# Performance work log

Measured on AMD Instinct MI355X. Metric: run time of the kernel, lower is better.

Reference implementation:

```python
import jax, jax.numpy as jnp
import numpy as np

H = 16
INPUT_DIM = 1024
FEATURE_DIM = 1024
HEAD_DIM = FEATURE_DIM // H


def setup_inputs() -> dict:
    key = jax.random.key(0)
    ks = jax.random.split(key, 12)
    B, S = 4, 2048
    s = 1.0 / np.sqrt(INPUT_DIM)
    inp = {
        "data": jax.random.normal(ks[0], (B, S, INPUT_DIM), dtype=jnp.float32),
        "context": jax.random.normal(ks[1], (B, S, INPUT_DIM), dtype=jnp.float32),
        "wq": jax.random.normal(ks[2], (INPUT_DIM, FEATURE_DIM), dtype=jnp.float32) * s,
        "bq": jnp.zeros((FEATURE_DIM,), dtype=jnp.float32),
        "wk": jax.random.normal(ks[3], (INPUT_DIM, FEATURE_DIM), dtype=jnp.float32) * s,
        "bk": jnp.zeros((FEATURE_DIM,), dtype=jnp.float32),
        "wv": jax.random.normal(ks[4], (INPUT_DIM, FEATURE_DIM), dtype=jnp.float32) * s,
        "bv": jnp.zeros((FEATURE_DIM,), dtype=jnp.float32),
        "wo": jax.random.normal(ks[5], (FEATURE_DIM, INPUT_DIM), dtype=jnp.float32) * s,
        "bo": jnp.zeros((INPUT_DIM,), dtype=jnp.float32),
    }
    return inp


def reference(data, context, wq, bq, wk, bk, wv, bv, wo, bo):
    B, S1, _ = data.shape
    S2 = context.shape[1]
    # QKV projections -> (B, H, S, head_dim)
    q = (data @ wq + bq).reshape(B, S1, H, HEAD_DIM).transpose(0, 2, 1, 3)
    k = (context @ wk + bk).reshape(B, S2, H, HEAD_DIM).transpose(0, 2, 1, 3)
    v = (context @ wv + bv).reshape(B, S2, H, HEAD_DIM).transpose(0, 2, 1, 3)
    scale = 1.0 / np.sqrt(HEAD_DIM).astype(np.float32)
    scores = jnp.einsum("bhqd,bhkd->bhqk", q, k) * scale  # (B,H,S1,S2)
    # causal mask (is_causal=True, S1>1): row >= col
    causal = jnp.arange(S1)[:, None] >= jnp.arange(S2)[None, :]
    scores = jnp.where(causal, scores, -jnp.inf)
    probs = jax.nn.softmax(scores, axis=-1)
    z = jnp.einsum("bhqk,bhkd->bhqd", probs, v)  # (B,H,S1,head_dim)
    z = z.transpose(0, 2, 1, 3).reshape(B, S1, FEATURE_DIM)
    return z @ wo + bo
```

## Files before the change

kernel.cpp:

```cpp
#include <hip/hip_runtime.h>
#include <hip/hip_bf16.h>
#include <math.h>

typedef short  short8  __attribute__((ext_vector_type(8)));
typedef short  short4_ __attribute__((ext_vector_type(4)));
typedef float  f32x4   __attribute__((ext_vector_type(4)));

__device__ __forceinline__ unsigned short f2bf(float f) {
  unsigned int u = __float_as_uint(f);
  u += 0x7fffu + ((u >> 16) & 1u);
  return (unsigned short)(u >> 16);
}

__device__ __forceinline__ float fexp2(float x) {
  float r;
  asm("v_exp_f32 %0, %1" : "=v"(r) : "v"(x));
  return r;
}

__device__ __forceinline__ void load_lds16(const void* g, void* l) {
  __builtin_amdgcn_global_load_lds(
      (const __attribute__((address_space(1))) unsigned int*)g,
      (__attribute__((address_space(3))) unsigned int*)l, 16, 0, 0);
}

__device__ __forceinline__ void store_out(float* p, float v) { *p = v; }
__device__ __forceinline__ void store_out(unsigned short* p, float v) { *p = f2bf(v); }

__global__ void k_cvt(const float* __restrict__ in, unsigned short* __restrict__ out, int n) {
  int i = (blockIdx.x * blockDim.x + threadIdx.x) * 8;
  if (i >= n) return;
  const float4* p = (const float4*)(in + i);
  float4 a = p[0], b = p[1];
  union { short8 v; unsigned short s[8]; } o;
  o.s[0] = f2bf(a.x); o.s[1] = f2bf(a.y); o.s[2] = f2bf(a.z); o.s[3] = f2bf(a.w);
  o.s[4] = f2bf(b.x); o.s[5] = f2bf(b.y); o.s[6] = f2bf(b.z); o.s[7] = f2bf(b.w);
  *(short8*)(out + i) = o.v;
}

__global__ void k_cvtT(const float* __restrict__ in, unsigned short* __restrict__ out) {
  __shared__ float tile[64][65];
  const int k0 = blockIdx.y * 64, n0 = blockIdx.x * 64;
  const int t = threadIdx.x;
  const int tr = t >> 6, tc = t & 63;
  #pragma unroll
  for (int i = 0; i < 16; i++) {
    int r = i * 4 + tr;
    tile[r][tc] = in[(size_t)(k0 + r) * 1024 + n0 + tc];
  }
  __syncthreads();
  #pragma unroll
  for (int i = 0; i < 16; i++) {
    int r = i * 4 + tr;
    out[(size_t)(n0 + r) * 1024 + k0 + tc] = f2bf(tile[tc][r]);
  }
}

template <typename OutT, bool BIAS_ROW>
__global__ __launch_bounds__(256) void k_gemm(
    const unsigned short* __restrict__ A,
    const unsigned short* __restrict__ Bt,
    const float* __restrict__ bias,
    OutT* __restrict__ C, int M, int N, int K, int NBX, float oscale)
{
  __shared__ unsigned short Als[128 * 64];
  __shared__ unsigned short Bls[128 * 64];
  const int t = threadIdx.x, lane = t & 63, w = t >> 6;
  const int wm = w >> 1, wn = w & 1;
  const int cpx = gridDim.x >> 3;
  const int id2 = (blockIdx.x & 7) * cpx + (blockIdx.x >> 3);
  const int m0 = (id2 / NBX) * 128, n0 = (id2 % NBX) * 128;
  const int l4 = lane >> 4, l15 = lane & 15;

  f32x4 acc[4][4];
  #pragma unroll
  for (int i = 0; i < 4; i++)
    #pragma unroll
    for (int j = 0; j < 4; j++) acc[i][j] = (f32x4){0.f, 0.f, 0.f, 0.f};

  for (int kk = 0; kk < K; kk += 64) {
    __syncthreads();
    #pragma unroll
    for (int i = 0; i < 4; i++) {
      int chunk = w * 256 + i * 64 + lane;
      int row = chunk >> 3, slot = chunk & 7;
      int ss = slot ^ (row & 7);
      load_lds16(A + (size_t)(m0 + row) * K + kk + ss * 8, &Als[chunk * 8]);
      load_lds16(Bt + (size_t)(n0 + row) * K + kk + ss * 8, &Bls[chunk * 8]);
    }
    __syncthreads();
    #pragma unroll
    for (int ks = 0; ks < 2; ks++) {
      short8 af[4], bf[4];
      #pragma unroll
      for (int m = 0; m < 4; m++) {
        int row = wm * 64 + m * 16 + l15;
        int sl = (ks * 4 + l4) ^ (row & 7);
        af[m] = *(const short8*)&Als[row * 64 + sl * 8];
      }
      #pragma unroll
      for (int n = 0; n < 4; n++) {
        int row = wn * 64 + n * 16 + l15;
        int sl = (ks * 4 + l4) ^ (row & 7);
        bf[n] = *(const short8*)&Bls[row * 64 + sl * 8];
      }
      #pragma unroll
      for (int m = 0; m < 4; m++)
        #pragma unroll
        for (int n = 0; n < 4; n++)
          acc[m][n] = __builtin_amdgcn_mfma_f32_16x16x32_bf16(af[m], bf[n], acc[m][n], 0, 0, 0);
    }
  }
  #pragma unroll
  for (int m = 0; m < 4; m++)
    #pragma unroll
    for (int r = 0; r < 4; r++) {
      int row = m0 + wm * 64 + m * 16 + l4 * 4 + r;
      #pragma unroll
      for (int n = 0; n < 4; n++) {
        int col = n0 + wn * 64 + n * 16 + l15;
        float v = (acc[m][n][r] + (BIAS_ROW ? bias[row] : bias[col])) * oscale;
        store_out(&C[(size_t)row * N + col], v);
      }
    }
}

__global__ __launch_bounds__(256, 4) void k_attn(
    const unsigned short* __restrict__ Q,
    const unsigned short* __restrict__ Km,
    const unsigned short* __restrict__ Vt,
    unsigned short* __restrict__ Z)
{
  __shared__ __align__(16) unsigned short Kls[2][64 * 64];
  __shared__ __align__(16) unsigned short Vls[2][64 * 64];
  const int t = threadIdx.x, lane = t & 63, w = t >> 6;
  const int l4 = lane >> 4, l15 = lane & 15;
  const int qt = 15 - (int)(blockIdx.x >> 6);
  const int bh = blockIdx.x & 63;
  const int h = bh & 15, b = bh >> 4;
  const int jend = 2 * qt + 1;
  const int wrow = qt * 128 + w * 32;
  const int jdiag = wrow >> 6;

  const int xr = l15 & 7;
  const int base0 = l15 * 64 + ((l4)     ^ xr) * 8;
  const int base1 = l15 * 64 + ((4 + l4) ^ xr) * 8;
  const unsigned short* Kp0 = &Kls[0][0] + base0;
  const unsigned short* Kp1 = &Kls[0][0] + base1;
  const char* Vc0; const char* Vc1; const char* Vc2; const char* Vc3;
  {
    const char* Vbase = (const char*)&Vls[0][0] + l15 * 128 + ((l4 & 1) << 3);
    const int a = l4 >> 1;
    Vc0 = Vbase + (((0 | a) ^ xr) << 4);
    Vc1 = Vbase + (((2 | a) ^ xr) << 4);
    Vc2 = Vbase + (((4 | a) ^ xr) << 4);
    Vc3 = Vbase + (((6 | a) ^ xr) << 4);
  }

  const int c0 = t, c1 = t + 256;
  const int r0 = c0 >> 3, s0 = (c0 & 7) ^ (r0 & 7);
  const int r1 = c1 >> 3, s1 = (c1 & 7) ^ (r1 & 7);
  const size_t kg0 = ((size_t)b * 2048 + r0) * 1024 + h * 64 + s0 * 8;
  const size_t kg1 = ((size_t)b * 2048 + r1) * 1024 + h * 64 + s1 * 8;
  const size_t vg0 = ((size_t)h * 64 + r0) * 8192 + (size_t)b * 2048 + s0 * 8;
  const size_t vg1 = ((size_t)h * 64 + r1) * 8192 + (size_t)b * 2048 + s1 * 8;

  #define STAGE(bb, j)                                                \
    do {                                                              \
      load_lds16(Km + kg0 + (size_t)(j) * 65536, &Kls[bb][c0 * 8]);   \
      load_lds16(Km + kg1 + (size_t)(j) * 65536, &Kls[bb][c1 * 8]);   \
      load_lds16(Vt + vg0 + (size_t)(j) * 64,    &Vls[bb][c0 * 8]);   \
      load_lds16(Vt + vg1 + (size_t)(j) * 64,    &Vls[bb][c1 * 8]);   \
    } while (0)

  short8 qfA[2], qfB[2];
  {
    size_t qrA = ((size_t)b * 2048 + wrow + l15) * 1024 + h * 64;
    size_t qrB = qrA + 16 * 1024;
    #pragma unroll
    for (int ks = 0; ks < 2; ks++) {
      qfA[ks] = *(const short8*)&Q[qrA + ks * 32 + l4 * 8];
      qfB[ks] = *(const short8*)&Q[qrB + ks * 32 + l4 * 8];
    }
  }
  short8 ones;
  #pragma unroll
  for (int i = 0; i < 8; i++) ones[i] = (short)0x3F80;
  const f32x4 zf = (f32x4){0.f, 0.f, 0.f, 0.f};

  f32x4 oaccA[4], oaccB[4], lsumA, lsumB;
  #pragma unroll
  for (int n = 0; n < 4; n++) {
    oaccA[n] = zf;
    oaccB[n] = zf;
  }
  lsumA = zf;
  lsumB = zf;

  STAGE(0, 0);
  asm volatile("s_waitcnt vmcnt(0)" ::: "memory");
  __syncthreads();

  auto SM = [&](f32x4 (&s)[4], int qbase, int j, bool diag, short8& pf0, short8& pf1) {
    if (diag) {
      const int q = qbase + l15;
      const int kb = j * 64 + l4 * 4;
      #pragma unroll
      for (int n = 0; n < 4; n++)
        #pragma unroll
        for (int r = 0; r < 4; r++)
          if (kb + n * 16 + r > q) s[n][r] = -__builtin_inff();
    }
    float p[4][4];
    #pragma unroll
    for (int n = 0; n < 4; n++)
      #pragma unroll
      for (int r = 0; r < 4; r++) p[n][r] = fexp2(s[n][r]);
    unsigned int lo0, hi0, lo1, hi1, lo2, hi2, lo3, hi3;
    asm("v_cvt_pk_bf16_f32 %0, %1, %2" : "=v"(lo0) : "v"(p[0][0]), "v"(p[0][1]));
    asm("v_cvt_pk_bf16_f32 %0, %1, %2" : "=v"(hi0) : "v"(p[0][2]), "v"(p[0][3]));
    asm("v_cvt_pk_bf16_f32 %0, %1, %2" : "=v"(lo1) : "v"(p[1][0]), "v"(p[1][1]));
    asm("v_cvt_pk_bf16_f32 %0, %1, %2" : "=v"(hi1) : "v"(p[1][2]), "v"(p[1][3]));
    asm("v_cvt_pk_bf16_f32 %0, %1, %2" : "=v"(lo2) : "v"(p[2][0]), "v"(p[2][1]));
    asm("v_cvt_pk_bf16_f32 %0, %1, %2" : "=v"(hi2) : "v"(p[2][2]), "v"(p[2][3]));
    asm("v_cvt_pk_bf16_f32 %0, %1, %2" : "=v"(lo3) : "v"(p[3][0]), "v"(p[3][1]));
    asm("v_cvt_pk_bf16_f32 %0, %1, %2" : "=v"(hi3) : "v"(p[3][2]), "v"(p[3][3]));
    union { unsigned int d[4]; short8 s8; } u0, u1;
    u0.d[0] = lo0; u0.d[1] = hi0; u0.d[2] = lo1; u0.d[3] = hi1;
    u1.d[0] = lo2; u1.d[1] = hi2; u1.d[2] = lo3; u1.d[3] = hi3;
    pf0 = u0.s8;
    pf1 = u1.s8;
  };

  int buf = 0;
  for (int j = 0; j <= jend; ++j) {
    if (j < jend) STAGE(buf ^ 1, j + 1);

    if (j * 64 <= wrow) {
      const unsigned short* Kb0 = Kp0 + buf * 4096;
      const unsigned short* Kb1 = Kp1 + buf * 4096;
      const int bo = buf * 8192;

      f32x4 sA[4], sB[4];
      __builtin_amdgcn_s_setprio(1);
      #pragma unroll
      for (int n = 0; n < 4; n++) {
        short8 kf = *(const short8*)(Kb0 + n * 1024);
        sA[n] = __builtin_amdgcn_mfma_f32_16x16x32_bf16(kf, qfA[0], zf, 0, 0, 0);
        sB[n] = __builtin_amdgcn_mfma_f32_16x16x32_bf16(kf, qfB[0], zf, 0, 0, 0);
      }
      #pragma unroll
      for (int n = 0; n < 4; n++) {
        short8 kf = *(const short8*)(Kb1 + n * 1024);
        sA[n] = __builtin_amdgcn_mfma_f32_16x16x32_bf16(kf, qfA[1], sA[n], 0, 0, 0);
        sB[n] = __builtin_amdgcn_mfma_f32_16x16x32_bf16(kf, qfB[1], sB[n], 0, 0, 0);
      }
      __builtin_amdgcn_s_setprio(0);

      const bool diag = (j == jdiag);
      short8 pfA0, pfA1, pfB0, pfB1;
      SM(sA, wrow,      j, diag, pfA0, pfA1);
      SM(sB, wrow + 16, j, diag, pfB0, pfB1);

      __builtin_amdgcn_s_setprio(1);
      lsumA = __builtin_amdgcn_mfma_f32_16x16x32_bf16(pfA0, ones, lsumA, 0, 0, 0);
      lsumB = __builtin_amdgcn_mfma_f32_16x16x32_bf16(pfB0, ones, lsumB, 0, 0, 0);
      #pragma unroll
      for (int n = 0; n < 4; n++) {
        union { short4_ h[2]; short8 s8; } vv;
        vv.h[0] = *(const short4_*)(Vc0 + bo + n * 2048);
        vv.h[1] = *(const short4_*)(Vc1 + bo + n * 2048);
        oaccA[n] = __builtin_amdgcn_mfma_f32_16x16x32_bf16(pfA0, vv.s8, oaccA[n], 0, 0, 0);
        oaccB[n] = __builtin_amdgcn_mfma_f32_16x16x32_bf16(pfB0, vv.s8, oaccB[n], 0, 0, 0);
      }
      lsumA = __builtin_amdgcn_mfma_f32_16x16x32_bf16(pfA1, ones, lsumA, 0, 0, 0);
      lsumB = __builtin_amdgcn_mfma_f32_16x16x32_bf16(pfB1, ones, lsumB, 0, 0, 0);
      #pragma unroll
      for (int n = 0; n < 4; n++) {
        union { short4_ h[2]; short8 s8; } vv;
        vv.h[0] = *(const short4_*)(Vc2 + bo + n * 2048);
        vv.h[1] = *(const short4_*)(Vc3 + bo + n * 2048);
        oaccA[n] = __builtin_amdgcn_mfma_f32_16x16x32_bf16(pfA1, vv.s8, oaccA[n], 0, 0, 0);
        oaccB[n] = __builtin_amdgcn_mfma_f32_16x16x32_bf16(pfB1, vv.s8, oaccB[n], 0, 0, 0);
      }
      __builtin_amdgcn_s_setprio(0);
    }

    asm volatile("s_waitcnt vmcnt(0)" ::: "memory");
    __syncthreads();
    buf ^= 1;
  }
  #undef STAGE

  #pragma unroll
  for (int r = 0; r < 4; r++) {
    float invA = 1.f / lsumA[r];
    float invB = 1.f / lsumB[r];
    size_t rowA = (size_t)b * 2048 + wrow + l4 * 4 + r;
    size_t rowB = rowA + 16;
    #pragma unroll
    for (int n = 0; n < 4; n++) {
      Z[rowA * 1024 + h * 64 + n * 16 + l15] = f2bf(oaccA[n][r] * invA);
      Z[rowB * 1024 + h * 64 + n * 16 + l15] = f2bf(oaccB[n][r] * invB);
    }
  }
}

extern "C" void kernel_launch(void* const* d_in, const int* in_sizes, int n_in,
                              void* d_out, int out_size, void* d_ws, size_t ws_size,
                              hipStream_t stream) {
  const float* data = (const float*)d_in[0];
  const float* context = (const float*)d_in[1];
  const float* wq = (const float*)d_in[2];
  const float* bq = (const float*)d_in[3];
  const float* wk = (const float*)d_in[4];
  const float* bk = (const float*)d_in[5];
  const float* wv = (const float*)d_in[6];
  const float* bv = (const float*)d_in[7];
  const float* wo = (const float*)d_in[8];
  const float* bo = (const float*)d_in[9];
  float* out = (float*)d_out;

  char* ws = (char*)d_ws;
  const size_t SZ_X = (size_t)8192 * 1024 * 2;
  const size_t SZ_W = (size_t)1024 * 1024 * 2;
  unsigned short* Xd  = (unsigned short*)(ws);
  unsigned short* Xc  = (unsigned short*)(ws + SZ_X);
  unsigned short* WqT = (unsigned short*)(ws + 2 * SZ_X);
  unsigned short* WkT = (unsigned short*)(ws + 2 * SZ_X + SZ_W);
  unsigned short* WvT = (unsigned short*)(ws + 2 * SZ_X + 2 * SZ_W);
  unsigned short* WoT = (unsigned short*)(ws + 2 * SZ_X + 3 * SZ_W);
  unsigned short* Qm  = (unsigned short*)(ws + 2 * SZ_X + 4 * SZ_W);
  unsigned short* Km  = (unsigned short*)(ws + 3 * SZ_X + 4 * SZ_W);
  unsigned short* Vt  = (unsigned short*)(ws + 4 * SZ_X + 4 * SZ_W);
  unsigned short* Zm  = (unsigned short*)(ws + 5 * SZ_X + 4 * SZ_W);

  const int NX = 8192 * 1024;
  k_cvt<<<NX / (256 * 8), 256, 0, stream>>>(data, Xd, NX);
  k_cvt<<<NX / (256 * 8), 256, 0, stream>>>(context, Xc, NX);
  k_cvtT<<<dim3(16, 16), 256, 0, stream>>>(wq, WqT);
  k_cvtT<<<dim3(16, 16), 256, 0, stream>>>(wk, WkT);
  k_cvtT<<<dim3(16, 16), 256, 0, stream>>>(wv, WvT);
  k_cvtT<<<dim3(16, 16), 256, 0, stream>>>(wo, WoT);

  const float SC = 0.125f * 1.44269504f;
  k_gemm<unsigned short, false><<<512, 256, 0, stream>>>(Xd, WqT, bq, Qm, 8192, 1024, 1024, 8, SC);
  k_gemm<unsigned short, false><<<512, 256, 0, stream>>>(Xc, WkT, bk, Km, 8192, 1024, 1024, 8, 1.0f);
  k_gemm<unsigned short, true><<<512, 256, 0, stream>>>(WvT, Xc, bv, Vt, 1024, 8192, 1024, 64, 1.0f);

  k_attn<<<1024, 256, 0, stream>>>(Qm, Km, Vt, Zm);

  k_gemm<float, false><<<512, 256, 0, stream>>>(Zm, WoT, bo, out, 8192, 1024, 1024, 8, 1.0f);
}
```

Measured before the change: 178.0 us.

## Give each attention wave 64 query rows with two waves per block

The attention kernel drops from four waves per block to two, and each wave now owns 64 query rows (four 16-row fragments) instead of 32. Each K/V fragment read from LDS then feeds four MFMA streams instead of two, which halves LDS reads per unit of compute. Staging loads are spread over fewer threads. The cost is much higher register pressure (16 output accumulators plus scores per wave), fewer waves to hide latency, and coarser causal skipping, since a wave now covers a whole 64-row key tile.

Result: slower. 186.8 us (+5.0%).

```diff
diff --git a/kernel.cpp b/kernel.cpp
--- a/kernel.cpp
+++ b/kernel.cpp
@@ -125,7 +125,7 @@
     }
 }
 
-__global__ __launch_bounds__(256, 4) void k_attn(
+__global__ __launch_bounds__(128, 2) void k_attn(
     const unsigned short* __restrict__ Q,
     const unsigned short* __restrict__ Km,
     const unsigned short* __restrict__ Vt,
@@ -139,7 +139,7 @@
   const int bh = blockIdx.x & 63;
   const int h = bh & 15, b = bh >> 4;
   const int jend = 2 * qt + 1;
-  const int wrow = qt * 128 + w * 32;
+  const int wrow = qt * 128 + w * 64;
   const int jdiag = wrow >> 6;
 
   const int xr = l15 & 7;
@@ -157,45 +157,52 @@
     Vc3 = Vbase + (((6 | a) ^ xr) << 4);
   }
 
-  const int c0 = t, c1 = t + 256;
+  const int c0 = t, c1 = t + 128, c2 = t + 256, c3 = t + 384;
   const int r0 = c0 >> 3, s0 = (c0 & 7) ^ (r0 & 7);
   const int r1 = c1 >> 3, s1 = (c1 & 7) ^ (r1 & 7);
+  const int r2 = c2 >> 3, s2 = (c2 & 7) ^ (r2 & 7);
+  const int r3 = c3 >> 3, s3 = (c3 & 7) ^ (r3 & 7);
   const size_t kg0 = ((size_t)b * 2048 + r0) * 1024 + h * 64 + s0 * 8;
   const size_t kg1 = ((size_t)b * 2048 + r1) * 1024 + h * 64 + s1 * 8;
+  const size_t kg2 = ((size_t)b * 2048 + r2) * 1024 + h * 64 + s2 * 8;
+  const size_t kg3 = ((size_t)b * 2048 + r3) * 1024 + h * 64 + s3 * 8;
   const size_t vg0 = ((size_t)h * 64 + r0) * 8192 + (size_t)b * 2048 + s0 * 8;
   const size_t vg1 = ((size_t)h * 64 + r1) * 8192 + (size_t)b * 2048 + s1 * 8;
+  const size_t vg2 = ((size_t)h * 64 + r2) * 8192 + (size_t)b * 2048 + s2 * 8;
+  const size_t vg3 = ((size_t)h * 64 + r3) * 8192 + (size_t)b * 2048 + s3 * 8;
 
   #define STAGE(bb, j)                                                \
     do {                                                              \
       load_lds16(Km + kg0 + (size_t)(j) * 65536, &Kls[bb][c0 * 8]);   \
       load_lds16(Km + kg1 + (size_t)(j) * 65536, &Kls[bb][c1 * 8]);   \
+      load_lds16(Km + kg2 + (size_t)(j) * 65536, &Kls[bb][c2 * 8]);   \
+      load_lds16(Km + kg3 + (size_t)(j) * 65536, &Kls[bb][c3 * 8]);   \
       load_lds16(Vt + vg0 + (size_t)(j) * 64,    &Vls[bb][c0 * 8]);   \
       load_lds16(Vt + vg1 + (size_t)(j) * 64,    &Vls[bb][c1 * 8]);   \
+      load_lds16(Vt + vg2 + (size_t)(j) * 64,    &Vls[bb][c2 * 8]);   \
+      load_lds16(Vt + vg3 + (size_t)(j) * 64,    &Vls[bb][c3 * 8]);   \
     } while (0)
 
-  short8 qfA[2], qfB[2];
-  {
-    size_t qrA = ((size_t)b * 2048 + wrow + l15) * 1024 + h * 64;
-    size_t qrB = qrA + 16 * 1024;
-    #pragma unroll
-    for (int ks = 0; ks < 2; ks++) {
-      qfA[ks] = *(const short8*)&Q[qrA + ks * 32 + l4 * 8];
-      qfB[ks] = *(const short8*)&Q[qrB + ks * 32 + l4 * 8];
-    }
+  short8 qf[4][2];
+  #pragma unroll
+  for (int f = 0; f < 4; f++) {
+    size_t qr = ((size_t)b * 2048 + wrow + f * 16 + l15) * 1024 + h * 64;
+    #pragma unroll
+    for (int ks = 0; ks < 2; ks++)
+      qf[f][ks] = *(const short8*)&Q[qr + ks * 32 + l4 * 8];
   }
   short8 ones;
   #pragma unroll
   for (int i = 0; i < 8; i++) ones[i] = (short)0x3F80;
   const f32x4 zf = (f32x4){0.f, 0.f, 0.f, 0.f};
 
-  f32x4 oaccA[4], oaccB[4], lsumA, lsumB;
-  #pragma unroll
-  for (int n = 0; n < 4; n++) {
-    oaccA[n] = zf;
-    oaccB[n] = zf;
-  }
-  lsumA = zf;
-  lsumB = zf;
+  f32x4 oacc[4][4], lsum[4];
+  #pragma unroll
+  for (int f = 0; f < 4; f++) {
+    lsum[f] = zf;
+    #pragma unroll
+    for (int n = 0; n < 4; n++) oacc[f][n] = zf;
+  }
 
   STAGE(0, 0);
   asm volatile("s_waitcnt vmcnt(0)" ::: "memory");
@@ -241,47 +248,55 @@
       const unsigned short* Kb1 = Kp1 + buf * 4096;
       const int bo = buf * 8192;
 
-      f32x4 sA[4], sB[4];
+      f32x4 s[4][4];
       __builtin_amdgcn_s_setprio(1);
       #pragma unroll
       for (int n = 0; n < 4; n++) {
         short8 kf = *(const short8*)(Kb0 + n * 1024);
-        sA[n] = __builtin_amdgcn_mfma_f32_16x16x32_bf16(kf, qfA[0], zf, 0, 0, 0);
-        sB[n] = __builtin_amdgcn_mfma_f32_16x16x32_bf16(kf, qfB[0], zf, 0, 0, 0);
+        #pragma unroll
+        for (int f = 0; f < 4; f++)
+          s[f][n] = __builtin_amdgcn_mfma_f32_16x16x32_bf16(kf, qf[f][0], zf, 0, 0, 0);
       }
       #pragma unroll
       for (int n = 0; n < 4; n++) {
         short8 kf = *(const short8*)(Kb1 + n * 1024);
-        sA[n] = __builtin_amdgcn_mfma_f32_16x16x32_bf16(kf, qfA[1], sA[n], 0, 0, 0);
-        sB[n] = __builtin_amdgcn_mfma_f32_16x16x32_bf16(kf, qfB[1], sB[n], 0, 0, 0);
+        #pragma unroll
+        for (int f = 0; f < 4; f++)
+          s[f][n] = __builtin_amdgcn_mfma_f32_16x16x32_bf16(kf, qf[f][1], s[f][n], 0, 0, 0);
       }
       __builtin_amdgcn_s_setprio(0);
 
       const bool diag = (j == jdiag);
-      short8 pfA0, pfA1, pfB0, pfB1;
-      SM(sA, wrow,      j, diag, pfA0, pfA1);
-      SM(sB, wrow + 16, j, diag, pfB0, pfB1);
+      short8 pf[4][2];
+      SM(s[0], wrow,      j, diag, pf[0][0], pf[0][1]);
+      SM(s[1], wrow + 16, j, diag, pf[1][0], pf[1][1]);
+      SM(s[2], wrow + 32, j, diag, pf[2][0], pf[2][1]);
+      SM(s[3], wrow + 48, j, diag, pf[3][0], pf[3][1]);
 
       __builtin_amdgcn_s_setprio(1);
-      lsumA = __builtin_amdgcn_mfma_f32_16x16x32_bf16(pfA0, ones, lsumA, 0, 0, 0);
-      lsumB = __builtin_amdgcn_mfma_f32_16x16x32_bf16(pfB0, ones, lsumB, 0, 0, 0);
+      #pragma unroll
+      for (int f = 0; f < 4; f++)
+        lsum[f] = __builtin_amdgcn_mfma_f32_16x16x32_bf16(pf[f][0], ones, lsum[f], 0, 0, 0);
       #pragma unroll
       for (int n = 0; n < 4; n++) {
         union { short4_ h[2]; short8 s8; } vv;
         vv.h[0] = *(const short4_*)(Vc0 + bo + n * 2048);
         vv.h[1] = *(const short4_*)(Vc1 + bo + n * 2048);
-        oaccA[n] = __builtin_amdgcn_mfma_f32_16x16x32_bf16(pfA0, vv.s8, oaccA[n], 0, 0, 0);
-        oaccB[n] = __builtin_amdgcn_mfma_f32_16x16x32_bf16(pfB0, vv.s8, oaccB[n], 0, 0, 0);
-      }
-      lsumA = __builtin_amdgcn_mfma_f32_16x16x32_bf16(pfA1, ones, lsumA, 0, 0, 0);
-      lsumB = __builtin_amdgcn_mfma_f32_16x16x32_bf16(pfB1, ones, lsumB, 0, 0, 0);
+        #pragma unroll
+        for (int f = 0; f < 4; f++)
+          oacc[f][n] = __builtin_amdgcn_mfma_f32_16x16x32_bf16(pf[f][0], vv.s8, oacc[f][n], 0, 0, 0);
+      }
+      #pragma unroll
+      for (int f = 0; f < 4; f++)
+        lsum[f] = __builtin_amdgcn_mfma_f32_16x16x32_bf16(pf[f][1], ones, lsum[f], 0, 0, 0);
       #pragma unroll
       for (int n = 0; n < 4; n++) {
         union { short4_ h[2]; short8 s8; } vv;
         vv.h[0] = *(const short4_*)(Vc2 + bo + n * 2048);
         vv.h[1] = *(const short4_*)(Vc3 + bo + n * 2048);
-        oaccA[n] = __builtin_amdgcn_mfma_f32_16x16x32_bf16(pfA1, vv.s8, oaccA[n], 0, 0, 0);
-        oaccB[n] = __builtin_amdgcn_mfma_f32_16x16x32_bf16(pfB1, vv.s8, oaccB[n], 0, 0, 0);
+        #pragma unroll
+        for (int f = 0; f < 4; f++)
+          oacc[f][n] = __builtin_amdgcn_mfma_f32_16x16x32_bf16(pf[f][1], vv.s8, oacc[f][n], 0, 0, 0);
       }
       __builtin_amdgcn_s_setprio(0);
     }
@@ -293,17 +308,15 @@
   #undef STAGE
 
   #pragma unroll
-  for (int r = 0; r < 4; r++) {
-    float invA = 1.f / lsumA[r];
-    float invB = 1.f / lsumB[r];
-    size_t rowA = (size_t)b * 2048 + wrow + l4 * 4 + r;
-    size_t rowB = rowA + 16;
-    #pragma unroll
-    for (int n = 0; n < 4; n++) {
-      Z[rowA * 1024 + h * 64 + n * 16 + l15] = f2bf(oaccA[n][r] * invA);
-      Z[rowB * 1024 + h * 64 + n * 16 + l15] = f2bf(oaccB[n][r] * invB);
-    }
-  }
+  for (int f = 0; f < 4; f++)
+    #pragma unroll
+    for (int r = 0; r < 4; r++) {
+      float inv = 1.f / lsum[f][r];
+      size_t row = (size_t)b * 2048 + wrow + f * 16 + l4 * 4 + r;
+      #pragma unroll
+      for (int n = 0; n < 4; n++)
+        Z[row * 1024 + h * 64 + n * 16 + l15] = f2bf(oacc[f][n][r] * inv);
+    }
 }
 
 extern "C" void kernel_launch(void* const* d_in, const int* in_sizes, int n_in,
@@ -348,7 +361,7 @@
   k_gemm<unsigned short, false><<<512, 256, 0, stream>>>(Xc, WkT, bk, Km, 8192, 1024, 1024, 8, 1.0f);
   k_gemm<unsigned short, true><<<512, 256, 0, stream>>>(WvT, Xc, bv, Vt, 1024, 8192, 1024, 64, 1.0f);
 
-  k_attn<<<1024, 256, 0, stream>>>(Qm, Km, Vt, Zm);
+  k_attn<<<1024, 128, 0, stream>>>(Qm, Km, Vt, Zm);
 
   k_gemm<float, false><<<512, 256, 0, stream>>>(Zm, WoT, bo, out, 8192, 1024, 1024, 8, 1.0f);
 }
```
